# Kernel optimization log

Hardware: AMD Instinct MI355X
Metric: run time of the kernel (lower is better)

Reference implementation:

```python
import jax, jax.numpy as jnp
import numpy as np
from jax import lax

EPS = 2.220446049250313e-16  # sys.float_info.epsilon
PATCH, STRIDE, SAMPLE = 7, 3, 80
H_WEIGHT, LAMBDA_OCC, T_THR = 2.0, 0.05, 1.0


def _patches(x):
    # [N, C, H, W] -> [N, C*PATCH*PATCH, Ho, Wo]  (torch F.unfold equivalent; channel-dim
    # ordering is irrelevant because all downstream ops reduce over the channel dim)
    return lax.conv_general_dilated_patches(x, (PATCH, PATCH), (STRIDE, STRIDE), 'VALID')


def _grid_sample_nearest(feat, field):
    # feat [N, C, H, W]; field [N, Hs, Ws, 2] in [-1, 1]; align_corners=False, nearest
    N, C, H, W = feat.shape
    gx, gy = field[..., 0], field[..., 1]
    ix = jnp.clip(jnp.round(((gx + 1.0) * W - 1.0) * 0.5).astype(jnp.int32), 0, W - 1)
    iy = jnp.clip(jnp.round(((gy + 1.0) * H - 1.0) * 0.5).astype(jnp.int32), 0, H - 1)
    return jax.vmap(lambda f, y, x_: f[:, y, x_])(feat, iy, ix)  # [N, C, Hs, Ws]


def _extract(feature, field01):
    f = _patches(feature)
    return _grid_sample_nearest(f, field01 * 2.0 - 1.0)


def _cosine_distance(x, y):
    # x, y: [N, C, S, S]
    N, C = x.shape[:2]
    y_mean = y.reshape(N, C, -1).mean(-1)[:, :, None, None]

    def _norm(v):
        return v / (jnp.linalg.norm(v, ord=2, axis=1, keepdims=True) + EPS)

    xf = _norm(x - y_mean).reshape(N, C, -1)  # [N, C, P]
    yf = _norm(y - y_mean).reshape(N, C, -1)
    sim = jnp.einsum('ncp,ncq->npq', xf, yf)  # [N, P, P]
    return jnp.maximum((1.0 - sim) * 0.5, 0.0)


def _agc_loss(target_features, refer_features, target_field, refer_field):
    tfeat = _extract(target_features, target_field)
    rfeat = _extract(refer_features, refer_field)
    d = _cosine_distance(tfeat, rfeat)  # [N, P1, P2]
    P1, P2 = d.shape[1], d.shape[2]

    # occurrence reweighting (no-grad): count how often each refer patch is a nearest match
    idx0 = jnp.argmin(d[0], axis=-1)  # [P1]
    counts = jax.ops.segment_sum(jnp.ones((P1,), jnp.float32), idx0, num_segments=P2)
    thr = counts.max() * T_THR
    omega = P1 / P2
    occur = jnp.where((counts > 0) & (counts <= thr), counts / omega, 0.0)
    d = d + lax.stop_gradient(occur)[None, None, :] * LAMBDA_OCC

    d_min = d.min(axis=-1, keepdims=True)
    w = jnp.exp((1.0 - d / (d_min + EPS)) * H_WEIGHT)
    A = w / w.sum(axis=-1, keepdims=True)
    CX = A.max(axis=-1)
    return -jnp.log(CX).mean()


def setup_inputs() -> dict:
    key = jax.random.key(0)
    k1, k2, k3, k4 = jax.random.split(key, 4)
    return {
        'target_features': jax.random.uniform(k1, (1, 1, 512, 512), dtype=jnp.float32),
        'refer_features': jax.random.uniform(k2, (1, 1, 512, 512), dtype=jnp.float32),
        'target_field': jax.random.uniform(k3, (1, SAMPLE, SAMPLE, 2), dtype=jnp.float32),
        'refer_field': jax.random.uniform(k4, (1, SAMPLE, SAMPLE, 2), dtype=jnp.float32),
        'args': 0,
    }


def reference(target_features, refer_features, target_field, refer_field, args):
    del args  # unused, as in the torch module
    return _agc_loss(target_features, refer_features, target_field, refer_field)
```

## Files before the change

### kernel.cpp

```cpp
#include <hip/hip_runtime.h>
#include <math.h>

#define P      6400
#define K      49
#define KP     64
#define FH     169
#define IMG    512
#define EPSF   2.220446049250313e-16f
#define HWT    2.0f
#define LOCC   0.05f

#define CSPLIT 50
#define QCHUNK (P / CSPLIT)

typedef __attribute__((ext_vector_type(8))) short bf16x8;
typedef __attribute__((ext_vector_type(4))) float f32x4;

__device__ inline unsigned bfbits(float x)
{
    unsigned u = __float_as_uint(x);
    return (u + 0x7FFFu + ((u >> 16) & 1u)) >> 16;
}

__global__ void k_prep(const float* __restrict__ rf, const float* __restrict__ rfield,
                       float* __restrict__ ypart,
                       unsigned long long* __restrict__ packed1,
                       int* __restrict__ counts, unsigned* __restrict__ mbits,
                       int* __restrict__ tickets)
{
    int t = threadIdx.x;
    int gid = blockIdx.x * 256 + t;

    if (gid < P) {
        packed1[gid] = 0xFFFFFFFFFFFFFFFFULL;
        counts[gid]  = 0;
        mbits[gid]   = 0xFFFFFFFFu;
    }
    if (gid < 2) tickets[gid] = 0;

    int c = gid / P;
    int p = gid - c * P;
    float fx = rfield[p * 2 + 0];
    float fy = rfield[p * 2 + 1];
    float gx = fx * 2.0f - 1.0f;
    float gy = fy * 2.0f - 1.0f;
    int ix = (int)rintf(((gx + 1.0f) * (float)FH - 1.0f) * 0.5f);
    int iy = (int)rintf(((gy + 1.0f) * (float)FH - 1.0f) * 0.5f);
    ix = min(max(ix, 0), FH - 1);
    iy = min(max(iy, 0), FH - 1);
    int ky = c / 7, kx = c - ky * 7;
    float v = rf[(iy * 3 + ky) * IMG + (ix * 3 + kx)];

    float s = v;
#pragma unroll
    for (int m = 1; m < 64; m <<= 1) s += __shfl_xor(s, m, 64);
    __shared__ float acc4[4];
    int l = t & 63, w = t >> 6;
    if (l == 0) acc4[w] = s;
    __syncthreads();
    if (t == 0) ypart[c * 25 + (p >> 8)] = acc4[0] + acc4[1] + acc4[2] + acc4[3];
}

__global__ void k_normpack(const float* __restrict__ tf, const float* __restrict__ rf,
                           const float* __restrict__ tfield, const float* __restrict__ rfield,
                           const float* __restrict__ ypart,
                           unsigned short* __restrict__ tb, unsigned short* __restrict__ rb)
{
    __shared__ float ym[K];
    int t = threadIdx.x;
    if (t < K) {
        float s = 0.f;
#pragma unroll
        for (int i = 0; i < 25; ++i) s += ypart[t * 25 + i];
        ym[t] = s * (1.0f / (float)P);
    }
    __syncthreads();

    int gid = blockIdx.x * 256 + t;
    int sel = gid >= P;
    int p = sel ? gid - P : gid;
    const float* field = sel ? rfield : tfield;
    const float* feat  = sel ? rf : tf;
    unsigned short* ob = sel ? rb : tb;

    float fx = field[p * 2 + 0];
    float fy = field[p * 2 + 1];
    float gx = fx * 2.0f - 1.0f;
    float gy = fy * 2.0f - 1.0f;
    int ix = (int)rintf(((gx + 1.0f) * (float)FH - 1.0f) * 0.5f);
    int iy = (int)rintf(((gy + 1.0f) * (float)FH - 1.0f) * 0.5f);
    ix = min(max(ix, 0), FH - 1);
    iy = min(max(iy, 0), FH - 1);
    const float* base = feat + (iy * 3) * IMG + ix * 3;

    float v[K];
#pragma unroll
    for (int ky = 0; ky < 7; ++ky)
#pragma unroll
        for (int kx = 0; kx < 7; ++kx)
            v[ky * 7 + kx] = base[ky * IMG + kx];

    float ss = 0.f;
#pragma unroll
    for (int c = 0; c < K; ++c) {
        float x = v[c] - ym[c];
        v[c] = x;
        ss += x * x;
    }
    float rn = 1.0f / (sqrtf(ss) + EPSF);

    unsigned wbuf[KP / 2];
#pragma unroll
    for (int i = 0; i < KP / 2; ++i) {
        int c0 = 2 * i, c1 = 2 * i + 1;
        float x0 = (c0 < K) ? v[c0] * rn : 0.f;
        float x1 = (c1 < K) ? v[c1] * rn : 0.f;
        wbuf[i] = (bfbits(x1) << 16) | bfbits(x0);
    }
    uint4* o = (uint4*)(ob + p * KP);
#pragma unroll
    for (int i = 0; i < KP / 8; ++i)
        o[i] = make_uint4(wbuf[4 * i], wbuf[4 * i + 1], wbuf[4 * i + 2], wbuf[4 * i + 3]);
}

template<int MODE>
__global__ __launch_bounds__(256, 4)
void k_sweep(const unsigned short* __restrict__ tb, const unsigned short* __restrict__ rb,
             const int* __restrict__ counts, const unsigned* __restrict__ mbits_in,
             unsigned long long* __restrict__ packed1, unsigned* __restrict__ mbits_out,
             float* __restrict__ Spart)
{
    __shared__ uint4 bs[1024];
    const int p0 = blockIdx.x * 128, q0 = blockIdx.y * QCHUNK;
    const int t  = threadIdx.x;
    const int w  = t >> 6, l = t & 63;
    const int l15 = l & 15, lg = l >> 4;

    bf16x8 afr[2][2];
#pragma unroll
    for (int mt = 0; mt < 2; ++mt)
#pragma unroll
        for (int ks = 0; ks < 2; ++ks)
            afr[mt][ks] = *(const bf16x8*)(tb + (p0 + w * 32 + mt * 16 + l15) * KP + ks * 32 + lg * 8);

    {
        const int r = t >> 1;
        const int cbase = (t & 1) * 4;
        const uint4* src = (const uint4*)(rb + (q0 + r) * KP);
#pragma unroll
        for (int i = 0; i < 4; ++i) {
            int c = cbase + i;
            bs[r * 8 + (c ^ (r & 7))] = src[c];
        }
    }
    __syncthreads();

    f32x4 acc[2][8];
#pragma unroll
    for (int mt = 0; mt < 2; ++mt)
#pragma unroll
        for (int qt = 0; qt < 8; ++qt) acc[mt][qt] = (f32x4){0.f, 0.f, 0.f, 0.f};

#pragma unroll
    for (int qt = 0; qt < 8; ++qt) {
        const int row = qt * 16 + l15;
        bf16x8 b0 = *(const bf16x8*)&bs[row * 8 + ((0 + lg) ^ (row & 7))];
        bf16x8 b1 = *(const bf16x8*)&bs[row * 8 + ((4 + lg) ^ (row & 7))];
#pragma unroll
        for (int mt = 0; mt < 2; ++mt) {
            acc[mt][qt] = __builtin_amdgcn_mfma_f32_16x16x32_bf16(afr[mt][0], b0, acc[mt][qt], 0, 0, 0);
            acc[mt][qt] = __builtin_amdgcn_mfma_f32_16x16x32_bf16(afr[mt][1], b1, acc[mt][qt], 0, 0, 0);
        }
    }

    float osv[8];
    if (MODE >= 2) {
#pragma unroll
        for (int qt = 0; qt < 8; ++qt) osv[qt] = (float)counts[q0 + qt * 16 + l15] * LOCC;
    }

#pragma unroll
    for (int mt = 0; mt < 2; ++mt) {
#pragma unroll
        for (int r = 0; r < 4; ++r) {
            int p = p0 + w * 32 + mt * 16 + lg * 4 + r;
            float rinv = 0.f;
            if (MODE == 3) rinv = 1.0f / (__uint_as_float(mbits_in[p]) + EPSF);

            float bv = 1e30f; int bi = 0; float s = 0.f;
#pragma unroll
            for (int qt = 0; qt < 8; ++qt) {
                float d = fmaxf((1.0f - acc[mt][qt][r]) * 0.5f, 0.0f);
                if (MODE >= 2) d += osv[qt];
                if (MODE == 1) {
                    bool upd = d < bv;
                    bi = upd ? (q0 + qt * 16 + l15) : bi;
                    bv = upd ? d : bv;
                } else if (MODE == 2) {
                    bv = fminf(bv, d);
                } else {
                    s += __expf((1.0f - d * rinv) * HWT);
                }
            }

            if (MODE == 1) {
                unsigned long long enc =
                    ((unsigned long long)__float_as_uint(bv) << 32) | (unsigned)bi;
#pragma unroll
                for (int m = 1; m < 16; m <<= 1) {
                    unsigned long long o = __shfl_xor(enc, m, 64);
                    enc = (o < enc) ? o : enc;
                }
                if (l15 == 0) atomicMin(&packed1[p], enc);
            } else if (MODE == 2) {
#pragma unroll
                for (int m = 1; m < 16; m <<= 1) bv = fminf(bv, __shfl_xor(bv, m, 64));
                if (l15 == 0) atomicMin(&mbits_out[p], __float_as_uint(bv));
            } else {
#pragma unroll
                for (int m = 1; m < 16; m <<= 1) s += __shfl_xor(s, m, 64);
                if (l15 == 0) Spart[blockIdx.y * P + p] = s;
            }
        }
    }
}

__global__ void k_hist(const unsigned long long* __restrict__ packed1,
                       int* __restrict__ counts)
{
    int p = blockIdx.x * blockDim.x + threadIdx.x;
    if (p < P) atomicAdd(&counts[(unsigned)(packed1[p] & 0xffffffffULL)], 1);
}

__global__ void k_loss(const float* __restrict__ Spart, const unsigned* __restrict__ mbits,
                       float* __restrict__ partial, int* __restrict__ ticket,
                       float* __restrict__ out)
{
    int b = blockIdx.x, t = threadIdx.x;
    int p = b * 128 + t;
    float s = 0.f;
#pragma unroll
    for (int cb = 0; cb < CSPLIT; ++cb) s += Spart[cb * P + p];
    float m = __uint_as_float(mbits[p]);
    float lw = (1.0f - m / (m + EPSF)) * HWT;
    float v = logf(s) - lw;
    __shared__ float red[128];
    red[t] = v; __syncthreads();
    for (int w = 64; w > 0; w >>= 1) { if (t < w) red[t] += red[t + w]; __syncthreads(); }

    __shared__ int lastblk;
    if (t == 0) {
        atomicExch(&partial[b], red[0]);
        __threadfence();
        lastblk = (atomicAdd(ticket, 1) == CSPLIT - 1);
    }
    __syncthreads();
    if (lastblk && t < 64) {
        float x = (t < CSPLIT) ? atomicAdd(&partial[t], 0.0f) : 0.f;
#pragma unroll
        for (int mm = 32; mm > 0; mm >>= 1) x += __shfl_down(x, mm, 64);
        if (t == 0) out[0] = x * (1.0f / (float)P);
    }
}

extern "C" void kernel_launch(void* const* d_in, const int* in_sizes, int n_in,
                              void* d_out, int out_size, void* d_ws, size_t ws_size,
                              hipStream_t stream)
{
    const float* tf  = (const float*)d_in[0];
    const float* rf  = (const float*)d_in[1];
    const float* tfd = (const float*)d_in[2];
    const float* rfd = (const float*)d_in[3];
    float* out = (float*)d_out;

    float* ws = (float*)d_ws;
    float* ypart = ws;
    unsigned short* tb = (unsigned short*)(ws + 2048);
    unsigned short* rb = (unsigned short*)(ws + 206848);
    float* Spart = ws + 411648;
    unsigned long long* packed1 = (unsigned long long*)(ws + 731648);
    int*      counts  = (int*)(ws + 744448);
    unsigned* mbits   = (unsigned*)(ws + 750848);
    float*    partial = ws + 757248;
    int*      tickets = (int*)(ws + 757312);

    k_prep<<<K * P / 256, 256, 0, stream>>>(rf, rfd, ypart, packed1, counts, mbits, tickets);
    k_normpack<<<2 * P / 256, 256, 0, stream>>>(tf, rf, tfd, rfd, ypart, tb, rb);

    dim3 g(P / 128, CSPLIT);
    k_sweep<1><<<g, 256, 0, stream>>>(tb, rb, nullptr, nullptr, packed1, nullptr, nullptr);
    k_hist<<<(P + 255) / 256, 256, 0, stream>>>(packed1, counts);
    k_sweep<2><<<g, 256, 0, stream>>>(tb, rb, counts, nullptr, nullptr, mbits, nullptr);
    k_sweep<3><<<g, 256, 0, stream>>>(tb, rb, counts, mbits, nullptr, nullptr, Spart);

    k_loss<<<CSPLIT, 128, 0, stream>>>(Spart, mbits, partial, &tickets[1], out);
}
```

Measured before the change: 69.19 us.

## Fuse sweep passes into row-owning kernels, drop hist and loss kernels

```diff
diff --git a/kernel.cpp b/kernel.cpp
--- a/kernel.cpp
+++ b/kernel.cpp
@@ -10,8 +10,9 @@
 #define HWT    2.0f
 #define LOCC   0.05f
 
-#define CSPLIT 50
-#define QCHUNK (P / CSPLIT)
+#define CSPLIT   50
+#define NROWBLK  (P / 32)
+#define FXSCALE  1099511627776.0
 
 typedef __attribute__((ext_vector_type(8))) short bf16x8;
 typedef __attribute__((ext_vector_type(4))) float f32x4;
@@ -22,21 +23,51 @@
     return (u + 0x7FFFu + ((u >> 16) & 1u)) >> 16;
 }
 
+__device__ __forceinline__ void load_b(const unsigned short* __restrict__ rb,
+                                       int qc, int w, int l15, int lg,
+                                       bf16x8 (&b)[2][2])
+{
+#pragma unroll
+    for (int n = 0; n < 2; ++n) {
+        int q = qc * 128 + (w + n * 4) * 16 + l15;
+#pragma unroll
+        for (int ks = 0; ks < 2; ++ks)
+            b[n][ks] = *(const bf16x8*)(rb + q * KP + ks * 32 + lg * 8);
+    }
+}
+
+__device__ __forceinline__ void load_c(const int* __restrict__ counts,
+                                       int qc, int w, int l15, float (&c)[2])
+{
+#pragma unroll
+    for (int n = 0; n < 2; ++n)
+        c[n] = (float)counts[qc * 128 + (w + n * 4) * 16 + l15] * LOCC;
+}
+
+__device__ __forceinline__ void gemm_chunk(const bf16x8 (&a)[2][2],
+                                           const bf16x8 (&b)[2][2],
+                                           f32x4 (&acc)[2][2])
+{
+#pragma unroll
+    for (int mt = 0; mt < 2; ++mt)
+#pragma unroll
+        for (int n = 0; n < 2; ++n) {
+            f32x4 c = (f32x4){0.f, 0.f, 0.f, 0.f};
+            c = __builtin_amdgcn_mfma_f32_16x16x32_bf16(a[mt][0], b[n][0], c, 0, 0, 0);
+            c = __builtin_amdgcn_mfma_f32_16x16x32_bf16(a[mt][1], b[n][1], c, 0, 0, 0);
+            acc[mt][n] = c;
+        }
+}
+
 __global__ void k_prep(const float* __restrict__ rf, const float* __restrict__ rfield,
-                       float* __restrict__ ypart,
-                       unsigned long long* __restrict__ packed1,
-                       int* __restrict__ counts, unsigned* __restrict__ mbits,
-                       int* __restrict__ tickets)
+                       float* __restrict__ ypart, int* __restrict__ counts,
+                       unsigned long long* __restrict__ accum, int* __restrict__ ticket)
 {
     int t = threadIdx.x;
     int gid = blockIdx.x * 256 + t;
 
-    if (gid < P) {
-        packed1[gid] = 0xFFFFFFFFFFFFFFFFULL;
-        counts[gid]  = 0;
-        mbits[gid]   = 0xFFFFFFFFu;
-    }
-    if (gid < 2) tickets[gid] = 0;
+    if (gid < P) counts[gid] = 0;
+    if (gid == 0) { accum[0] = 0ULL; ticket[0] = 0; }
 
     int c = gid / P;
     int p = gid - c * P;
@@ -76,7 +107,7 @@
     }
     __syncthreads();
 
-    int gid = blockIdx.x * 256 + t;
+    int gid = blockIdx.x * 64 + t;
     int sel = gid >= P;
     int p = sel ? gid - P : gid;
     const float* field = sel ? rfield : tfield;
@@ -123,15 +154,11 @@
         o[i] = make_uint4(wbuf[4 * i], wbuf[4 * i + 1], wbuf[4 * i + 2], wbuf[4 * i + 3]);
 }
 
-template<int MODE>
-__global__ __launch_bounds__(256, 4)
-void k_sweep(const unsigned short* __restrict__ tb, const unsigned short* __restrict__ rb,
-             const int* __restrict__ counts, const unsigned* __restrict__ mbits_in,
-             unsigned long long* __restrict__ packed1, unsigned* __restrict__ mbits_out,
-             float* __restrict__ Spart)
-{
-    __shared__ uint4 bs[1024];
-    const int p0 = blockIdx.x * 128, q0 = blockIdx.y * QCHUNK;
+__global__ void k_rowmin(const unsigned short* __restrict__ tb,
+                         const unsigned short* __restrict__ rb,
+                         int* __restrict__ counts)
+{
+    const int p0 = blockIdx.x * 32;
     const int t  = threadIdx.x;
     const int w  = t >> 6, l = t & 63;
     const int l15 = l & 15, lg = l >> 4;
@@ -141,125 +168,199 @@
     for (int mt = 0; mt < 2; ++mt)
 #pragma unroll
         for (int ks = 0; ks < 2; ++ks)
-            afr[mt][ks] = *(const bf16x8*)(tb + (p0 + w * 32 + mt * 16 + l15) * KP + ks * 32 + lg * 8);
+            afr[mt][ks] = *(const bf16x8*)(tb + (p0 + mt * 16 + l15) * KP + ks * 32 + lg * 8);
+
+    unsigned long long enc[2][4];
+#pragma unroll
+    for (int mt = 0; mt < 2; ++mt)
+#pragma unroll
+        for (int r = 0; r < 4; ++r) enc[mt][r] = 0xFFFFFFFFFFFFFFFFULL;
+
+    bf16x8 bf0[2][2], bf1[2][2];
+    load_b(rb, 0, w, l15, lg, bf0);
+    for (int qc = 0; qc < CSPLIT; ++qc) {
+        if (qc + 1 < CSPLIT) load_b(rb, qc + 1, w, l15, lg, bf1);
+        f32x4 acc[2][2];
+        gemm_chunk(afr, bf0, acc);
+        const int qa = qc * 128 + w * 16 + l15;
+#pragma unroll
+        for (int mt = 0; mt < 2; ++mt)
+#pragma unroll
+            for (int r = 0; r < 4; ++r) {
+                float d0 = fmaxf((1.0f - acc[mt][0][r]) * 0.5f, 0.0f);
+                float d1 = fmaxf((1.0f - acc[mt][1][r]) * 0.5f, 0.0f);
+                bool sw = d1 < d0;
+                float dm = sw ? d1 : d0;
+                unsigned qi = (unsigned)(sw ? qa + 64 : qa);
+                unsigned long long e =
+                    ((unsigned long long)__float_as_uint(dm) << 32) | qi;
+                enc[mt][r] = e < enc[mt][r] ? e : enc[mt][r];
+            }
+#pragma unroll
+        for (int n = 0; n < 2; ++n)
+#pragma unroll
+            for (int ks = 0; ks < 2; ++ks) bf0[n][ks] = bf1[n][ks];
+    }
+
+    __shared__ unsigned long long wminU[4][32];
+#pragma unroll
+    for (int mt = 0; mt < 2; ++mt)
+#pragma unroll
+        for (int r = 0; r < 4; ++r) {
+            unsigned long long e = enc[mt][r];
+#pragma unroll
+            for (int m = 1; m < 16; m <<= 1) {
+                unsigned long long o = __shfl_xor(e, m, 64);
+                e = o < e ? o : e;
+            }
+            if (l15 == 0) wminU[w][mt * 16 + lg * 4 + r] = e;
+        }
+    __syncthreads();
+    if (t < 32) {
+        unsigned long long e = wminU[0][t];
+        e = wminU[1][t] < e ? wminU[1][t] : e;
+        e = wminU[2][t] < e ? wminU[2][t] : e;
+        e = wminU[3][t] < e ? wminU[3][t] : e;
+        atomicAdd(&counts[(unsigned)(e & 0xffffffffu)], 1);
+    }
+}
+
+__global__ void k_sweep23(const unsigned short* __restrict__ tb,
+                          const unsigned short* __restrict__ rb,
+                          const int* __restrict__ counts,
+                          unsigned long long* __restrict__ accum,
+                          int* __restrict__ ticket,
+                          float* __restrict__ out)
+{
+    const int p0 = blockIdx.x * 32;
+    const int t  = threadIdx.x;
+    const int w  = t >> 6, l = t & 63;
+    const int l15 = l & 15, lg = l >> 4;
+
+    __shared__ float wred[4][32];
+    __shared__ float dminS[32];
+    __shared__ float vv[32];
+
+    bf16x8 afr[2][2];
+#pragma unroll
+    for (int mt = 0; mt < 2; ++mt)
+#pragma unroll
+        for (int ks = 0; ks < 2; ++ks)
+            afr[mt][ks] = *(const bf16x8*)(tb + (p0 + mt * 16 + l15) * KP + ks * 32 + lg * 8);
+
+    float bv[2][4];
+#pragma unroll
+    for (int mt = 0; mt < 2; ++mt)
+#pragma unroll
+        for (int r = 0; r < 4; ++r) bv[mt][r] = 1e30f;
 
     {
-        const int r = t >> 1;
-        const int cbase = (t & 1) * 4;
-        const uint4* src = (const uint4*)(rb + (q0 + r) * KP);
-#pragma unroll
-        for (int i = 0; i < 4; ++i) {
-            int c = cbase + i;
-            bs[r * 8 + (c ^ (r & 7))] = src[c];
-        }
-    }
-    __syncthreads();
-
-    f32x4 acc[2][8];
-#pragma unroll
-    for (int mt = 0; mt < 2; ++mt)
-#pragma unroll
-        for (int qt = 0; qt < 8; ++qt) acc[mt][qt] = (f32x4){0.f, 0.f, 0.f, 0.f};
-
-#pragma unroll
-    for (int qt = 0; qt < 8; ++qt) {
-        const int row = qt * 16 + l15;
-        bf16x8 b0 = *(const bf16x8*)&bs[row * 8 + ((0 + lg) ^ (row & 7))];
-        bf16x8 b1 = *(const bf16x8*)&bs[row * 8 + ((4 + lg) ^ (row & 7))];
-#pragma unroll
-        for (int mt = 0; mt < 2; ++mt) {
-            acc[mt][qt] = __builtin_amdgcn_mfma_f32_16x16x32_bf16(afr[mt][0], b0, acc[mt][qt], 0, 0, 0);
-            acc[mt][qt] = __builtin_amdgcn_mfma_f32_16x16x32_bf16(afr[mt][1], b1, acc[mt][qt], 0, 0, 0);
-        }
-    }
-
-    float osv[8];
-    if (MODE >= 2) {
-#pragma unroll
-        for (int qt = 0; qt < 8; ++qt) osv[qt] = (float)counts[q0 + qt * 16 + l15] * LOCC;
-    }
-
-#pragma unroll
-    for (int mt = 0; mt < 2; ++mt) {
+        bf16x8 bf0[2][2], bf1[2][2]; float c0[2], c1[2];
+        load_b(rb, 0, w, l15, lg, bf0); load_c(counts, 0, w, l15, c0);
+        for (int qc = 0; qc < CSPLIT; ++qc) {
+            if (qc + 1 < CSPLIT) {
+                load_b(rb, qc + 1, w, l15, lg, bf1);
+                load_c(counts, qc + 1, w, l15, c1);
+            }
+            f32x4 acc[2][2];
+            gemm_chunk(afr, bf0, acc);
+#pragma unroll
+            for (int mt = 0; mt < 2; ++mt)
+#pragma unroll
+                for (int r = 0; r < 4; ++r) {
+                    float d0 = fmaxf((1.0f - acc[mt][0][r]) * 0.5f, 0.0f) + c0[0];
+                    float d1 = fmaxf((1.0f - acc[mt][1][r]) * 0.5f, 0.0f) + c0[1];
+                    bv[mt][r] = fminf(bv[mt][r], fminf(d0, d1));
+                }
+#pragma unroll
+            for (int n = 0; n < 2; ++n)
+#pragma unroll
+                for (int ks = 0; ks < 2; ++ks) bf0[n][ks] = bf1[n][ks];
+            c0[0] = c1[0]; c0[1] = c1[1];
+        }
+    }
+
+#pragma unroll
+    for (int mt = 0; mt < 2; ++mt)
 #pragma unroll
         for (int r = 0; r < 4; ++r) {
-            int p = p0 + w * 32 + mt * 16 + lg * 4 + r;
-            float rinv = 0.f;
-            if (MODE == 3) rinv = 1.0f / (__uint_as_float(mbits_in[p]) + EPSF);
-
-            float bv = 1e30f; int bi = 0; float s = 0.f;
-#pragma unroll
-            for (int qt = 0; qt < 8; ++qt) {
-                float d = fmaxf((1.0f - acc[mt][qt][r]) * 0.5f, 0.0f);
-                if (MODE >= 2) d += osv[qt];
-                if (MODE == 1) {
-                    bool upd = d < bv;
-                    bi = upd ? (q0 + qt * 16 + l15) : bi;
-                    bv = upd ? d : bv;
-                } else if (MODE == 2) {
-                    bv = fminf(bv, d);
-                } else {
-                    s += __expf((1.0f - d * rinv) * HWT);
+            float e = bv[mt][r];
+#pragma unroll
+            for (int m = 1; m < 16; m <<= 1) e = fminf(e, __shfl_xor(e, m, 64));
+            if (l15 == 0) wred[w][mt * 16 + lg * 4 + r] = e;
+        }
+    __syncthreads();
+    if (t < 32)
+        dminS[t] = fminf(fminf(wred[0][t], wred[1][t]), fminf(wred[2][t], wred[3][t]));
+    __syncthreads();
+
+    float rv[2][4], sacc[2][4];
+#pragma unroll
+    for (int mt = 0; mt < 2; ++mt)
+#pragma unroll
+        for (int r = 0; r < 4; ++r) {
+            rv[mt][r] = 1.0f / (dminS[mt * 16 + lg * 4 + r] + EPSF);
+            sacc[mt][r] = 0.f;
+        }
+
+    {
+        bf16x8 bf0[2][2], bf1[2][2]; float c0[2], c1[2];
+        load_b(rb, 0, w, l15, lg, bf0); load_c(counts, 0, w, l15, c0);
+        for (int qc = 0; qc < CSPLIT; ++qc) {
+            if (qc + 1 < CSPLIT) {
+                load_b(rb, qc + 1, w, l15, lg, bf1);
+                load_c(counts, qc + 1, w, l15, c1);
+            }
+            f32x4 acc[2][2];
+            gemm_chunk(afr, bf0, acc);
+#pragma unroll
+            for (int mt = 0; mt < 2; ++mt)
+#pragma unroll
+                for (int r = 0; r < 4; ++r) {
+                    float d0 = fmaxf((1.0f - acc[mt][0][r]) * 0.5f, 0.0f) + c0[0];
+                    float d1 = fmaxf((1.0f - acc[mt][1][r]) * 0.5f, 0.0f) + c0[1];
+                    sacc[mt][r] += __expf((1.0f - d0 * rv[mt][r]) * HWT)
+                                 + __expf((1.0f - d1 * rv[mt][r]) * HWT);
                 }
-            }
-
-            if (MODE == 1) {
-                unsigned long long enc =
-                    ((unsigned long long)__float_as_uint(bv) << 32) | (unsigned)bi;
-#pragma unroll
-                for (int m = 1; m < 16; m <<= 1) {
-                    unsigned long long o = __shfl_xor(enc, m, 64);
-                    enc = (o < enc) ? o : enc;
-                }
-                if (l15 == 0) atomicMin(&packed1[p], enc);
-            } else if (MODE == 2) {
-#pragma unroll
-                for (int m = 1; m < 16; m <<= 1) bv = fminf(bv, __shfl_xor(bv, m, 64));
-                if (l15 == 0) atomicMin(&mbits_out[p], __float_as_uint(bv));
-            } else {
-#pragma unroll
-                for (int m = 1; m < 16; m <<= 1) s += __shfl_xor(s, m, 64);
-                if (l15 == 0) Spart[blockIdx.y * P + p] = s;
-            }
-        }
-    }
-}
-
-__global__ void k_hist(const unsigned long long* __restrict__ packed1,
-                       int* __restrict__ counts)
-{
-    int p = blockIdx.x * blockDim.x + threadIdx.x;
-    if (p < P) atomicAdd(&counts[(unsigned)(packed1[p] & 0xffffffffULL)], 1);
-}
-
-__global__ void k_loss(const float* __restrict__ Spart, const unsigned* __restrict__ mbits,
-                       float* __restrict__ partial, int* __restrict__ ticket,
-                       float* __restrict__ out)
-{
-    int b = blockIdx.x, t = threadIdx.x;
-    int p = b * 128 + t;
-    float s = 0.f;
-#pragma unroll
-    for (int cb = 0; cb < CSPLIT; ++cb) s += Spart[cb * P + p];
-    float m = __uint_as_float(mbits[p]);
-    float lw = (1.0f - m / (m + EPSF)) * HWT;
-    float v = logf(s) - lw;
-    __shared__ float red[128];
-    red[t] = v; __syncthreads();
-    for (int w = 64; w > 0; w >>= 1) { if (t < w) red[t] += red[t + w]; __syncthreads(); }
-
-    __shared__ int lastblk;
+#pragma unroll
+            for (int n = 0; n < 2; ++n)
+#pragma unroll
+                for (int ks = 0; ks < 2; ++ks) bf0[n][ks] = bf1[n][ks];
+            c0[0] = c1[0]; c0[1] = c1[1];
+        }
+    }
+
+#pragma unroll
+    for (int mt = 0; mt < 2; ++mt)
+#pragma unroll
+        for (int r = 0; r < 4; ++r) {
+            float e = sacc[mt][r];
+#pragma unroll
+            for (int m = 1; m < 16; m <<= 1) e += __shfl_xor(e, m, 64);
+            if (l15 == 0) wred[w][mt * 16 + lg * 4 + r] = e;
+        }
+    __syncthreads();
+
+    if (t < 32) {
+        float s = ((wred[0][t] + wred[1][t]) + wred[2][t]) + wred[3][t];
+        float m = dminS[t];
+        float lw = (1.0f - m / (m + EPSF)) * HWT;
+        vv[t] = logf(s) - lw;
+    }
+    __syncthreads();
     if (t == 0) {
-        atomicExch(&partial[b], red[0]);
-        __threadfence();
-        lastblk = (atomicAdd(ticket, 1) == CSPLIT - 1);
-    }
-    __syncthreads();
-    if (lastblk && t < 64) {
-        float x = (t < CSPLIT) ? atomicAdd(&partial[t], 0.0f) : 0.f;
-#pragma unroll
-        for (int mm = 32; mm > 0; mm >>= 1) x += __shfl_down(x, mm, 64);
-        if (t == 0) out[0] = x * (1.0f / (float)P);
+        float vsum = 0.f;
+#pragma unroll
+        for (int i = 0; i < 32; ++i) vsum += vv[i];
+        double sd = (double)vsum * FXSCALE;
+        long long fx = (long long)(sd + (sd >= 0.0 ? 0.5 : -0.5));
+        atomicAdd(accum, (unsigned long long)fx);
+        asm volatile("s_waitcnt vmcnt(0)" ::: "memory");
+        int tk = atomicAdd(ticket, 1);
+        if (tk == NROWBLK - 1) {
+            unsigned long long tot = atomicAdd(accum, 0ULL);
+            out[0] = (float)((double)(long long)tot * (1.0 / FXSCALE) / (double)P);
+        }
     }
 }
 
@@ -277,21 +378,12 @@
     float* ypart = ws;
     unsigned short* tb = (unsigned short*)(ws + 2048);
     unsigned short* rb = (unsigned short*)(ws + 206848);
-    float* Spart = ws + 411648;
-    unsigned long long* packed1 = (unsigned long long*)(ws + 731648);
-    int*      counts  = (int*)(ws + 744448);
-    unsigned* mbits   = (unsigned*)(ws + 750848);
-    float*    partial = ws + 757248;
-    int*      tickets = (int*)(ws + 757312);
-
-    k_prep<<<K * P / 256, 256, 0, stream>>>(rf, rfd, ypart, packed1, counts, mbits, tickets);
-    k_normpack<<<2 * P / 256, 256, 0, stream>>>(tf, rf, tfd, rfd, ypart, tb, rb);
-
-    dim3 g(P / 128, CSPLIT);
-    k_sweep<1><<<g, 256, 0, stream>>>(tb, rb, nullptr, nullptr, packed1, nullptr, nullptr);
-    k_hist<<<(P + 255) / 256, 256, 0, stream>>>(packed1, counts);
-    k_sweep<2><<<g, 256, 0, stream>>>(tb, rb, counts, nullptr, nullptr, mbits, nullptr);
-    k_sweep<3><<<g, 256, 0, stream>>>(tb, rb, counts, mbits, nullptr, nullptr, Spart);
-
-    k_loss<<<CSPLIT, 128, 0, stream>>>(Spart, mbits, partial, &tickets[1], out);
-}
+    int* counts = (int*)(ws + 411648);
+    unsigned long long* accum = (unsigned long long*)(ws + 418048);
+    int* ticket = (int*)(ws + 418050);
+
+    k_prep<<<K * P / 256, 256, 0, stream>>>(rf, rfd, ypart, counts, accum, ticket);
+    k_normpack<<<2 * P / 64, 64, 0, stream>>>(tf, rf, tfd, rfd, ypart, tb, rb);
+    k_rowmin<<<NROWBLK, 256, 0, stream>>>(tb, rb, counts);
+    k_sweep23<<<NROWBLK, 256, 0, stream>>>(tb, rb, counts, accum, ticket, out);
+}
```

Result: slower. 96.55 us (+39.5%).

## Double sweep block rows and accumulate row sums via fixed-point atomics

Applied to the files above, without the earlier changes.

```diff
diff --git a/kernel.cpp b/kernel.cpp
--- a/kernel.cpp
+++ b/kernel.cpp
@@ -11,7 +11,9 @@
 #define LOCC   0.05f
 
 #define CSPLIT 50
-#define QCHUNK (P / CSPLIT)
+#define QCHUNK  (P / CSPLIT)
+#define RROWS   256
+#define FXSCALE 1099511627776.0
 
 typedef __attribute__((ext_vector_type(8))) short bf16x8;
 typedef __attribute__((ext_vector_type(4))) float f32x4;
@@ -26,7 +28,8 @@
                        float* __restrict__ ypart,
                        unsigned long long* __restrict__ packed1,
                        int* __restrict__ counts, unsigned* __restrict__ mbits,
-                       int* __restrict__ tickets)
+                       unsigned long long* __restrict__ Ssum,
+                       int* __restrict__ ticket)
 {
     int t = threadIdx.x;
     int gid = blockIdx.x * 256 + t;
@@ -35,8 +38,9 @@
         packed1[gid] = 0xFFFFFFFFFFFFFFFFULL;
         counts[gid]  = 0;
         mbits[gid]   = 0xFFFFFFFFu;
-    }
-    if (gid < 2) tickets[gid] = 0;
+        Ssum[gid]    = 0ULL;
+    }
+    if (gid == 0) ticket[0] = 0;
 
     int c = gid / P;
     int p = gid - c * P;
@@ -124,14 +128,14 @@
 }
 
 template<int MODE>
-__global__ __launch_bounds__(256, 4)
+__global__ __launch_bounds__(512, 2)
 void k_sweep(const unsigned short* __restrict__ tb, const unsigned short* __restrict__ rb,
              const int* __restrict__ counts, const unsigned* __restrict__ mbits_in,
              unsigned long long* __restrict__ packed1, unsigned* __restrict__ mbits_out,
-             float* __restrict__ Spart)
+             unsigned long long* __restrict__ Ssum)
 {
     __shared__ uint4 bs[1024];
-    const int p0 = blockIdx.x * 128, q0 = blockIdx.y * QCHUNK;
+    const int p0 = blockIdx.x * RROWS, q0 = blockIdx.y * QCHUNK;
     const int t  = threadIdx.x;
     const int w  = t >> 6, l = t & 63;
     const int l15 = l & 15, lg = l >> 4;
@@ -144,11 +148,11 @@
             afr[mt][ks] = *(const bf16x8*)(tb + (p0 + w * 32 + mt * 16 + l15) * KP + ks * 32 + lg * 8);
 
     {
-        const int r = t >> 1;
-        const int cbase = (t & 1) * 4;
+        const int r = t >> 2;
+        const int cbase = (t & 3) * 2;
         const uint4* src = (const uint4*)(rb + (q0 + r) * KP);
 #pragma unroll
-        for (int i = 0; i < 4; ++i) {
+        for (int i = 0; i < 2; ++i) {
             int c = cbase + i;
             bs[r * 8 + (c ^ (r & 7))] = src[c];
         }
@@ -219,7 +223,10 @@
             } else {
 #pragma unroll
                 for (int m = 1; m < 16; m <<= 1) s += __shfl_xor(s, m, 64);
-                if (l15 == 0) Spart[blockIdx.y * P + p] = s;
+                if (l15 == 0) {
+                    double sd = (double)s * FXSCALE + 0.5;
+                    atomicAdd(&Ssum[p], (unsigned long long)sd);
+                }
             }
         }
     }
@@ -232,15 +239,14 @@
     if (p < P) atomicAdd(&counts[(unsigned)(packed1[p] & 0xffffffffULL)], 1);
 }
 
-__global__ void k_loss(const float* __restrict__ Spart, const unsigned* __restrict__ mbits,
+__global__ void k_loss(const unsigned long long* __restrict__ Ssum,
+                       const unsigned* __restrict__ mbits,
                        float* __restrict__ partial, int* __restrict__ ticket,
                        float* __restrict__ out)
 {
     int b = blockIdx.x, t = threadIdx.x;
     int p = b * 128 + t;
-    float s = 0.f;
-#pragma unroll
-    for (int cb = 0; cb < CSPLIT; ++cb) s += Spart[cb * P + p];
+    float s = (float)((double)Ssum[p] * (1.0 / FXSCALE));
     float m = __uint_as_float(mbits[p]);
     float lw = (1.0f - m / (m + EPSF)) * HWT;
     float v = logf(s) - lw;
@@ -277,21 +283,21 @@
     float* ypart = ws;
     unsigned short* tb = (unsigned short*)(ws + 2048);
     unsigned short* rb = (unsigned short*)(ws + 206848);
-    float* Spart = ws + 411648;
-    unsigned long long* packed1 = (unsigned long long*)(ws + 731648);
-    int*      counts  = (int*)(ws + 744448);
-    unsigned* mbits   = (unsigned*)(ws + 750848);
-    float*    partial = ws + 757248;
-    int*      tickets = (int*)(ws + 757312);
-
-    k_prep<<<K * P / 256, 256, 0, stream>>>(rf, rfd, ypart, packed1, counts, mbits, tickets);
-    k_normpack<<<2 * P / 256, 256, 0, stream>>>(tf, rf, tfd, rfd, ypart, tb, rb);
-
-    dim3 g(P / 128, CSPLIT);
-    k_sweep<1><<<g, 256, 0, stream>>>(tb, rb, nullptr, nullptr, packed1, nullptr, nullptr);
+    unsigned long long* packed1 = (unsigned long long*)(ws + 411648);
+    unsigned long long* Ssum    = (unsigned long long*)(ws + 424448);
+    unsigned* mbits   = (unsigned*)(ws + 437248);
+    int*      counts  = (int*)(ws + 443648);
+    float*    partial = ws + 450048;
+    int*      ticket  = (int*)(ws + 450112);
+
+    k_prep<<<K * P / 256, 256, 0, stream>>>(rf, rfd, ypart, packed1, counts, mbits, Ssum, ticket);
+    k_normpack<<<(2 * P + 255) / 256, 256, 0, stream>>>(tf, rf, tfd, rfd, ypart, tb, rb);
+
+    dim3 g(P / RROWS, CSPLIT);
+    k_sweep<1><<<g, 512, 0, stream>>>(tb, rb, nullptr, nullptr, packed1, nullptr, nullptr);
     k_hist<<<(P + 255) / 256, 256, 0, stream>>>(packed1, counts);
-    k_sweep<2><<<g, 256, 0, stream>>>(tb, rb, counts, nullptr, nullptr, mbits, nullptr);
-    k_sweep<3><<<g, 256, 0, stream>>>(tb, rb, counts, mbits, nullptr, nullptr, Spart);
-
-    k_loss<<<CSPLIT, 128, 0, stream>>>(Spart, mbits, partial, &tickets[1], out);
-}
+    k_sweep<2><<<g, 512, 0, stream>>>(tb, rb, counts, nullptr, nullptr, mbits, nullptr);
+    k_sweep<3><<<g, 512, 0, stream>>>(tb, rb, counts, mbits, nullptr, nullptr, Ssum);
+
+    k_loss<<<CSPLIT, 128, 0, stream>>>(Ssum, mbits, partial, ticket, out);
+}
```

Measured after the change: 73.78 us. 6.6% more time.
